# Kernel optimization log

Hardware: AMD Instinct MI355X
Metric: run time of the kernel (lower is better)

Reference implementation:

```python
import jax, jax.numpy as jnp
import numpy as np

DECAY = 0.99
EPS = 1e-05


def setup_inputs() -> dict:
    key = jax.random.key(0)
    k1, k2, k3 = jax.random.split(key, 3)
    N, K, D = 131072, 1024, 64
    return {
        "z": jax.random.normal(k1, (N, D), dtype=jnp.float32),
        "embeddings": jax.random.normal(k2, (K, D), dtype=jnp.float32),
        "cluster_size": jnp.ones((K,), dtype=jnp.float32),
        "ema_embed_sum": jax.random.normal(k3, (K, D), dtype=jnp.float32),
    }


def reference(z, embeddings, cluster_size, ema_embed_sum):
    # z: [N, D]; embeddings/ema_embed_sum: [K, D]; cluster_size: [K]
    N, D = z.shape
    K = embeddings.shape[0]

    # squared pairwise distances via the ||a||^2 - 2ab + ||b||^2 expansion
    d = (
        jnp.sum(z * z, axis=-1, keepdims=True)
        - 2.0 * (z @ embeddings.T)
        + jnp.sum(embeddings * embeddings, axis=-1)
    )  # [N, K]
    encoding_indices = jnp.argmin(d, axis=1)  # [N]
    z_q = embeddings[encoding_indices]  # [N, D]

    # EMA codebook update (training mode; one_hot.sum(0) == counts, one_hot.T @ z == segment_sum)
    counts = jax.ops.segment_sum(jnp.ones((N,), z.dtype), encoding_indices, num_segments=K)
    new_cluster_size = cluster_size * DECAY + (1.0 - DECAY) * counts
    embed_sum = jax.ops.segment_sum(z, encoding_indices, num_segments=K)  # [K, D]
    new_ema_embed_sum = ema_embed_sum * DECAY + (1.0 - DECAY) * embed_sum
    n = jnp.sum(new_cluster_size)
    cs = (new_cluster_size + EPS) / (n + K * EPS) * n
    new_embeddings = new_ema_embed_sum / cs[:, None]

    commitment_loss = jnp.mean((z - z_q) ** 2)
    z_q_st = z + jax.lax.stop_gradient(z_q - z)  # value == z_q
    return (z_q_st, commitment_loss, encoding_indices, new_embeddings, new_cluster_size, new_ema_embed_sum)
```

## Files before the change

### kernel.cpp

```cpp
#include <hip/hip_runtime.h>

#define N_PTS 131072
#define K_CODES 1024
#define DIM 64
#define DECAYF 0.99f
#define OMDF 0.01f
#define EPSF 1e-5f
#define TAU 0.0625f

#define OUT_ZQ      0
#define OUT_LOSS    8388608
#define OUT_IDX     8388609
#define OUT_NEWEMB  8519681
#define OUT_NEWCS   8585217
#define OUT_NEWEMA  8586241

#define WS_C8       0
#define WS_ACNT     8192
#define WS_EMBSUM   8208
#define WS_ZERO_END 73744
#define WS_ENORM    73744
#define WS_CNT      74768
#define WS_START    75792
#define WS_CUR8     76816
#define WS_LOSSARR  85008
#define WS_CS       85520
#define WS_AMBIG    86544
#define WS_ORDER    217616
#define WS_E2       348688

typedef __attribute__((ext_vector_type(8))) short bf16x8;
typedef __attribute__((ext_vector_type(4))) float f32x4;

static __device__ inline short f2bf(float f) {
    unsigned u = __float_as_uint(f);
    unsigned r = (u + 0x7fffu + ((u >> 16) & 1u)) >> 16;
    return (short)r;
}
static __device__ inline float bf2f(short h) {
    return __uint_as_float(((unsigned)(unsigned short)h) << 16);
}

__global__ __launch_bounds__(256) void econv_kernel(const float* __restrict__ E,
                                                    short* __restrict__ E2,
                                                    float* __restrict__ enorm) {
    int k = blockIdx.x * 256 + threadIdx.x;
    const float* ep = E + (size_t)k * DIM;
    short* o = E2 + (size_t)k * 128;
    float s = 0.f;
#pragma unroll
    for (int d = 0; d < 64; ++d) {
        float f = ep[d];
        s += f * f;
        float m = -2.f * f;
        short h = f2bf(m);
        o[d] = h;
        o[64 + d] = f2bf(m - bf2f(h));
    }
    enorm[k] = s;
}

__global__ __launch_bounds__(256) void argmin_mfma(const float* __restrict__ z,
                                                   const short* __restrict__ E2,
                                                   const float* __restrict__ enorm,
                                                   float* __restrict__ out_idx_f,
                                                   float* __restrict__ counts8,
                                                   int* __restrict__ ambig_cnt,
                                                   int* __restrict__ ambig) {
    int tid = threadIdx.x;
    int w = tid >> 6, lane = tid & 63;
    int c = lane & 15, q = lane >> 4;
    int mbase = blockIdx.x * 256 + w * 64;

    bf16x8 a[4][4];
#pragma unroll
    for (int t = 0; t < 4; ++t) {
        const float* zp = z + (size_t)(mbase + t * 16 + c) * DIM;
        const float4* z4a = (const float4*)(zp + q * 8);
        const float4* z4b = (const float4*)(zp + 32 + q * 8);
        float f[16];
        float4 v0 = z4a[0], v1 = z4a[1], v2 = z4b[0], v3 = z4b[1];
        f[0]=v0.x; f[1]=v0.y; f[2]=v0.z; f[3]=v0.w;
        f[4]=v1.x; f[5]=v1.y; f[6]=v1.z; f[7]=v1.w;
        f[8]=v2.x; f[9]=v2.y; f[10]=v2.z; f[11]=v2.w;
        f[12]=v3.x; f[13]=v3.y; f[14]=v3.z; f[15]=v3.w;
#pragma unroll
        for (int j = 0; j < 8; ++j) {
            short h0 = f2bf(f[j]);
            a[t][0][j] = h0;
            a[t][2][j] = f2bf(f[j] - bf2f(h0));
            short h1 = f2bf(f[8 + j]);
            a[t][1][j] = h1;
            a[t][3][j] = f2bf(f[8 + j] - bf2f(h1));
        }
    }

    float s1[16], s2[16];
    int i1[16];
#pragma unroll
    for (int idx = 0; idx < 16; ++idx) { s1[idx] = INFINITY; s2[idx] = INFINITY; i1[idx] = 0; }

    int vcode = c;
    for (int tile = 0; tile < 64; ++tile) {
        const bf16x8* bp = (const bf16x8*)E2 + ((size_t)(tile * 16 + c) * 16) + q;
        bf16x8 bh0 = bp[0], bh1 = bp[4], bl0 = bp[8], bl1 = bp[12];
        float en = enorm[tile * 16 + c];
#pragma unroll
        for (int t = 0; t < 4; ++t) {
            f32x4 acc = {0.f, 0.f, 0.f, 0.f};
            acc = __builtin_amdgcn_mfma_f32_16x16x32_bf16(a[t][0], bl0, acc, 0, 0, 0);
            acc = __builtin_amdgcn_mfma_f32_16x16x32_bf16(a[t][1], bl1, acc, 0, 0, 0);
            acc = __builtin_amdgcn_mfma_f32_16x16x32_bf16(a[t][2], bh0, acc, 0, 0, 0);
            acc = __builtin_amdgcn_mfma_f32_16x16x32_bf16(a[t][3], bh1, acc, 0, 0, 0);
            acc = __builtin_amdgcn_mfma_f32_16x16x32_bf16(a[t][0], bh0, acc, 0, 0, 0);
            acc = __builtin_amdgcn_mfma_f32_16x16x32_bf16(a[t][1], bh1, acc, 0, 0, 0);
#pragma unroll
            for (int i = 0; i < 4; ++i) {
                float s = en + acc[i];
                int idx = t * 4 + i;
                bool bl = s < s1[idx];
                s2[idx] = bl ? s1[idx] : fminf(s2[idx], s);
                i1[idx] = bl ? vcode : i1[idx];
                s1[idx] = bl ? s : s1[idx];
            }
        }
        vcode += 16;
    }

#pragma unroll
    for (int off = 1; off < 16; off <<= 1) {
#pragma unroll
        for (int idx = 0; idx < 16; ++idx) {
            float os1 = __shfl_xor(s1[idx], off);
            float os2 = __shfl_xor(s2[idx], off);
            int   oi1 = __shfl_xor(i1[idx], off);
            float ns2 = fminf(fmaxf(s1[idx], os1), fminf(s2[idx], os2));
            if (os1 < s1[idx]) { s1[idx] = os1; i1[idx] = oi1; }
            s2[idx] = ns2;
        }
    }

    if (c == 0) {
#pragma unroll
        for (int idx = 0; idx < 16; ++idx) {
            int t = idx >> 2, i = idx & 3;
            int row = mbase + t * 16 + q * 4 + i;
            int code = i1[idx];
            out_idx_f[row] = (float)code;
            if (s2[idx] - s1[idx] >= TAU) {
                atomicAdd(&counts8[(((unsigned)row >> 8) & 7) * K_CODES + code], 1.0f);
            } else {
                int p = atomicAdd(ambig_cnt, 1);
                ambig[p] = row;
            }
        }
    }
}

__global__ __launch_bounds__(256) void rescue_kernel(const float* __restrict__ z,
                                                     const float* __restrict__ E,
                                                     const float* __restrict__ enorm,
                                                     const int* __restrict__ ambig_cnt,
                                                     const int* __restrict__ ambig,
                                                     float* __restrict__ out_idx_f,
                                                     float* __restrict__ counts8) {
    int lane = threadIdx.x & 63;
    int wave = (blockIdx.x * 256 + threadIdx.x) >> 6;
    int nw = gridDim.x * 4;
    int cnt = *ambig_cnt;
    for (int a = 2 * wave; a < cnt; a += 2 * nw) {
        int row0 = ambig[a];
        bool two = (a + 1) < cnt;
        int row1 = two ? ambig[a + 1] : row0;
        const float4* zp0 = (const float4*)(z + (size_t)row0 * DIM);
        const float4* zp1 = (const float4*)(z + (size_t)row1 * DIM);
        float4 zr0[16], zr1[16];
#pragma unroll
        for (int i = 0; i < 16; ++i) { zr0[i] = zp0[i]; zr1[i] = zp1[i]; }
        float best0 = INFINITY, best1 = INFINITY;
        int bi0 = 0, bi1 = 0;
        for (int j = 0; j < 16; ++j) {
            int code = j * 64 + lane;
            const float4* ep = (const float4*)(E + (size_t)code * DIM);
            float a0 = 0.f, a1 = 0.f, a2 = 0.f, a3 = 0.f;
            float c0 = 0.f, c1 = 0.f, c2 = 0.f, c3 = 0.f;
#pragma unroll
            for (int i = 0; i < 16; ++i) {
                float4 ev = ep[i];
                a0 += zr0[i].x * ev.x; a1 += zr0[i].y * ev.y;
                a2 += zr0[i].z * ev.z; a3 += zr0[i].w * ev.w;
                c0 += zr1[i].x * ev.x; c1 += zr1[i].y * ev.y;
                c2 += zr1[i].z * ev.z; c3 += zr1[i].w * ev.w;
            }
            float en = enorm[code];
            float s0 = en - 2.f * ((a0 + a1) + (a2 + a3));
            float s1 = en - 2.f * ((c0 + c1) + (c2 + c3));
            if (s0 < best0) { best0 = s0; bi0 = code; }
            if (s1 < best1) { best1 = s1; bi1 = code; }
        }
#pragma unroll
        for (int off = 1; off < 64; off <<= 1) {
            float ob = __shfl_xor(best0, off);
            int oi = __shfl_xor(bi0, off);
            if (ob < best0 || (ob == best0 && oi < bi0)) { best0 = ob; bi0 = oi; }
            float ob1 = __shfl_xor(best1, off);
            int oi1 = __shfl_xor(bi1, off);
            if (ob1 < best1 || (ob1 == best1 && oi1 < bi1)) { best1 = ob1; bi1 = oi1; }
        }
        if (lane == 0) {
            out_idx_f[row0] = (float)bi0;
            atomicAdd(&counts8[(((unsigned)row0 >> 8) & 7) * K_CODES + bi0], 1.0f);
            if (two) {
                out_idx_f[row1] = (float)bi1;
                atomicAdd(&counts8[(((unsigned)row1 >> 8) & 7) * K_CODES + bi1], 1.0f);
            }
        }
    }
}

__global__ __launch_bounds__(256) void zq_loss_kernel(const float* __restrict__ z,
                                                      const float* __restrict__ E,
                                                      const float* __restrict__ idx_f,
                                                      float* __restrict__ zq,
                                                      float* __restrict__ lossarr) {
    __shared__ int s_k[256];
    __shared__ float red[256];
    int tid = threadIdx.x;
    int rbase = blockIdx.x * 256;
    s_k[tid] = (int)idx_f[rbase + tid];
    __syncthreads();
    float acc = 0.f;
    size_t ebase = (size_t)rbase * DIM;
    for (int it = 0; it < 64; ++it) {
        int le = it * 256 + tid;
        int rl = le >> 6, d = le & 63;
        float ev = E[(size_t)s_k[rl] * DIM + d];
        float zv = z[ebase + le];
        zq[ebase + le] = ev;
        float df = zv - ev;
        acc += df * df;
    }
    red[tid] = acc;
    __syncthreads();
    for (int st = 128; st > 0; st >>= 1) {
        if (tid < st) red[tid] += red[tid + st];
        __syncthreads();
    }
    if (tid == 0) lossarr[blockIdx.x] = red[0];
}

__global__ __launch_bounds__(1024) void scan_kernel(const float* __restrict__ cluster_size,
                                                    const float* __restrict__ counts8,
                                                    float* __restrict__ ncs_out,
                                                    float* __restrict__ cs_ws,
                                                    float* __restrict__ cnt_out,
                                                    int* __restrict__ start,
                                                    int* __restrict__ cursor8) {
    int k = threadIdx.x;
    float c8[8];
    float cnt = 0.f;
#pragma unroll
    for (int s = 0; s < 8; ++s) { c8[s] = counts8[s * K_CODES + k]; cnt += c8[s]; }
    cnt_out[k] = cnt;
    float ncs = cluster_size[k] * DECAYF + OMDF * cnt;
    ncs_out[k] = ncs;

    __shared__ float red[1024];
    __shared__ int pfx[1024];
    red[k] = ncs;
    pfx[k] = (int)cnt;
    __syncthreads();
    for (int st = 512; st > 0; st >>= 1) {
        if (k < st) red[k] += red[k + st];
        __syncthreads();
    }
    float n = red[0];
    cs_ws[k] = (ncs + EPSF) / (n + (float)K_CODES * EPSF) * n;

    int my = (int)cnt;
    for (int off = 1; off < 1024; off <<= 1) {
        int add = (k >= off) ? pfx[k - off] : 0;
        __syncthreads();
        pfx[k] += add;
        __syncthreads();
    }
    int excl = pfx[k] - my;
    start[k] = excl;
    int run = excl;
#pragma unroll
    for (int s = 0; s < 8; ++s) { cursor8[s * K_CODES + k] = run; run += (int)c8[s]; }
}

__global__ __launch_bounds__(256) void scatter_kernel(const float* __restrict__ idx_f,
                                                      int* __restrict__ cursor8,
                                                      int* __restrict__ order) {
    int row = blockIdx.x * 256 + threadIdx.x;
    int k = (int)idx_f[row];
    int shard = ((unsigned)row >> 8) & 7;
    int p = atomicAdd(&cursor8[shard * K_CODES + k], 1);
    order[p] = (k << 17) | row;
}

__global__ __launch_bounds__(256) void segsum_kernel(const float* __restrict__ z,
                                                     const int* __restrict__ order,
                                                     float* __restrict__ embsum) {
    int lane = threadIdx.x & 63;
    int w = threadIdx.x >> 6;
    int wave = blockIdx.x * 4 + w;
    int base = wave * 64;

    int my = order[base + lane];

    int cur = __shfl(my, 0, 64) >> 17;
    float sum = 0.f;
#pragma unroll 8
    for (int i = 0; i < 64; ++i) {
        int p = __shfl(my, i, 64);
        int row = p & 0x1FFFF;
        int code = p >> 17;
        float v = z[(size_t)row * DIM + lane];
        if (code != cur) {
            atomicAdd(&embsum[(size_t)cur * DIM + lane], sum);
            sum = 0.f;
            cur = code;
        }
        sum += v;
    }
    atomicAdd(&embsum[(size_t)cur * DIM + lane], sum);
}

__global__ __launch_bounds__(256) void ema2_kernel(const float* __restrict__ ema,
                                                   const float* __restrict__ embsum,
                                                   const float* __restrict__ cs_ws,
                                                   float* __restrict__ newema_out,
                                                   float* __restrict__ newemb_out) {
    int i = blockIdx.x * 256 + threadIdx.x;
    float nes = ema[i] * DECAYF + OMDF * embsum[i];
    newema_out[i] = nes;
    newemb_out[i] = nes / cs_ws[i >> 6];
}

__global__ __launch_bounds__(512) void finalize_kernel(const float* __restrict__ lossarr,
                                                       float* __restrict__ loss_out) {
    __shared__ float red[512];
    red[threadIdx.x] = lossarr[threadIdx.x];
    __syncthreads();
    for (int st = 256; st > 0; st >>= 1) {
        if (threadIdx.x < st) red[threadIdx.x] += red[threadIdx.x + st];
        __syncthreads();
    }
    if (threadIdx.x == 0)
        loss_out[0] = red[0] * (1.0f / ((float)N_PTS * (float)DIM));
}

extern "C" void kernel_launch(void* const* d_in, const int* in_sizes, int n_in,
                              void* d_out, int out_size, void* d_ws, size_t ws_size,
                              hipStream_t stream) {
    const float* z            = (const float*)d_in[0];
    const float* E            = (const float*)d_in[1];
    const float* cluster_size = (const float*)d_in[2];
    const float* ema          = (const float*)d_in[3];
    float* out = (float*)d_out;
    float* ws  = (float*)d_ws;

    hipMemsetAsync(ws, 0, (size_t)WS_ZERO_END * sizeof(float), stream);

    econv_kernel<<<4, 256, 0, stream>>>(E, (short*)(ws + WS_E2), ws + WS_ENORM);

    argmin_mfma<<<N_PTS / 256, 256, 0, stream>>>(z, (const short*)(ws + WS_E2),
                                                 ws + WS_ENORM,
                                                 out + OUT_IDX,
                                                 ws + WS_C8,
                                                 (int*)(ws + WS_ACNT),
                                                 (int*)(ws + WS_AMBIG));

    rescue_kernel<<<512, 256, 0, stream>>>(z, E, ws + WS_ENORM,
                                           (const int*)(ws + WS_ACNT),
                                           (const int*)(ws + WS_AMBIG),
                                           out + OUT_IDX,
                                           ws + WS_C8);

    zq_loss_kernel<<<N_PTS / 256, 256, 0, stream>>>(z, E, out + OUT_IDX,
                                                    out + OUT_ZQ,
                                                    ws + WS_LOSSARR);

    scan_kernel<<<1, 1024, 0, stream>>>(cluster_size, ws + WS_C8,
                                        out + OUT_NEWCS, ws + WS_CS,
                                        ws + WS_CNT,
                                        (int*)(ws + WS_START),
                                        (int*)(ws + WS_CUR8));

    scatter_kernel<<<N_PTS / 256, 256, 0, stream>>>(out + OUT_IDX,
                                                    (int*)(ws + WS_CUR8),
                                                    (int*)(ws + WS_ORDER));

    segsum_kernel<<<N_PTS / 256, 256, 0, stream>>>(z,
                                                   (const int*)(ws + WS_ORDER),
                                                   ws + WS_EMBSUM);

    ema2_kernel<<<K_CODES * DIM / 256, 256, 0, stream>>>(ema, ws + WS_EMBSUM,
                                                         ws + WS_CS,
                                                         out + OUT_NEWEMA,
                                                         out + OUT_NEWEMB);

    finalize_kernel<<<1, 512, 0, stream>>>(ws + WS_LOSSARR, out + OUT_LOSS);
}
```

Before: 263.1 us.

## Pack code index into distance bits, fuse loss into argmin, drop finalize

The argmin loop now packs the code index into the low 10 mantissa bits of each distance, folds the codebook norm into the MFMA accumulator init, and tracks the two smallest values with fmin/med3 instead of separate index selects. The commitment loss is computed as ||z||^2 plus the min distance inside argmin and rescue, summed with atomics, so the zq kernel no longer re-reads z and the finalize kernel is removed. The scan kernel switches to wave-shuffle prefix sums. The ambiguity threshold becomes magnitude-relative to cover the precision lost in the bit packing, and the loss is now derived from the bf16-split distance expansion, which risks numerical error.

```diff
diff --git a/kernel.cpp b/kernel.cpp
--- a/kernel.cpp
+++ b/kernel.cpp
@@ -6,7 +6,6 @@
 #define DECAYF 0.99f
 #define OMDF 0.01f
 #define EPSF 1e-5f
-#define TAU 0.0625f
 
 #define OUT_ZQ      0
 #define OUT_LOSS    8388608
@@ -17,17 +16,15 @@
 
 #define WS_C8       0
 #define WS_ACNT     8192
-#define WS_EMBSUM   8208
-#define WS_ZERO_END 73744
-#define WS_ENORM    73744
-#define WS_CNT      74768
-#define WS_START    75792
-#define WS_CUR8     76816
-#define WS_LOSSARR  85008
-#define WS_CS       85520
-#define WS_AMBIG    86544
-#define WS_ORDER    217616
-#define WS_E2       348688
+#define WS_LOSS     8208
+#define WS_EMBSUM   8224
+#define WS_ZERO_END 73760
+#define WS_ENORM    73760
+#define WS_CUR8     74784
+#define WS_CS       82976
+#define WS_AMBIG    84000
+#define WS_ORDER    215072
+#define WS_E2       346144
 
 typedef __attribute__((ext_vector_type(8))) short bf16x8;
 typedef __attribute__((ext_vector_type(4))) float f32x4;
@@ -66,13 +63,15 @@
                                                    float* __restrict__ out_idx_f,
                                                    float* __restrict__ counts8,
                                                    int* __restrict__ ambig_cnt,
-                                                   int* __restrict__ ambig) {
+                                                   int* __restrict__ ambig,
+                                                   float* __restrict__ loss_ws) {
     int tid = threadIdx.x;
     int w = tid >> 6, lane = tid & 63;
     int c = lane & 15, q = lane >> 4;
     int mbase = blockIdx.x * 256 + w * 64;
 
     bf16x8 a[4][4];
+    float znorm_t[4];
 #pragma unroll
     for (int t = 0; t < 4; ++t) {
         const float* zp = z + (size_t)(mbase + t * 16 + c) * DIM;
@@ -84,6 +83,12 @@
         f[4]=v1.x; f[5]=v1.y; f[6]=v1.z; f[7]=v1.w;
         f[8]=v2.x; f[9]=v2.y; f[10]=v2.z; f[11]=v2.w;
         f[12]=v3.x; f[13]=v3.y; f[14]=v3.z; f[15]=v3.w;
+        float zn = 0.f;
+#pragma unroll
+        for (int j = 0; j < 16; ++j) zn += f[j] * f[j];
+#pragma unroll
+        for (int off = 16; off < 64; off <<= 1) zn += __shfl_xor(zn, off);
+        znorm_t[t] = zn;
 #pragma unroll
         for (int j = 0; j < 8; ++j) {
             short h0 = f2bf(f[j]);
@@ -96,18 +101,17 @@
     }
 
     float s1[16], s2[16];
-    int i1[16];
-#pragma unroll
-    for (int idx = 0; idx < 16; ++idx) { s1[idx] = INFINITY; s2[idx] = INFINITY; i1[idx] = 0; }
-
-    int vcode = c;
+#pragma unroll
+    for (int idx = 0; idx < 16; ++idx) { s1[idx] = INFINITY; s2[idx] = INFINITY; }
+
+    unsigned vcode = (unsigned)c;
     for (int tile = 0; tile < 64; ++tile) {
         const bf16x8* bp = (const bf16x8*)E2 + ((size_t)(tile * 16 + c) * 16) + q;
         bf16x8 bh0 = bp[0], bh1 = bp[4], bl0 = bp[8], bl1 = bp[12];
         float en = enorm[tile * 16 + c];
 #pragma unroll
         for (int t = 0; t < 4; ++t) {
-            f32x4 acc = {0.f, 0.f, 0.f, 0.f};
+            f32x4 acc = {en, en, en, en};
             acc = __builtin_amdgcn_mfma_f32_16x16x32_bf16(a[t][0], bl0, acc, 0, 0, 0);
             acc = __builtin_amdgcn_mfma_f32_16x16x32_bf16(a[t][1], bl1, acc, 0, 0, 0);
             acc = __builtin_amdgcn_mfma_f32_16x16x32_bf16(a[t][2], bh0, acc, 0, 0, 0);
@@ -116,12 +120,12 @@
             acc = __builtin_amdgcn_mfma_f32_16x16x32_bf16(a[t][1], bh1, acc, 0, 0, 0);
 #pragma unroll
             for (int i = 0; i < 4; ++i) {
-                float s = en + acc[i];
+                float sp = __uint_as_float(
+                    (__float_as_uint(acc[i]) & 0xFFFFFC00u) | vcode);
                 int idx = t * 4 + i;
-                bool bl = s < s1[idx];
-                s2[idx] = bl ? s1[idx] : fminf(s2[idx], s);
-                i1[idx] = bl ? vcode : i1[idx];
-                s1[idx] = bl ? s : s1[idx];
+                float ns2 = __builtin_amdgcn_fmed3f(s1[idx], s2[idx], sp);
+                s1[idx] = fminf(s1[idx], sp);
+                s2[idx] = ns2;
             }
         }
         vcode += 16;
@@ -133,27 +137,48 @@
         for (int idx = 0; idx < 16; ++idx) {
             float os1 = __shfl_xor(s1[idx], off);
             float os2 = __shfl_xor(s2[idx], off);
-            int   oi1 = __shfl_xor(i1[idx], off);
-            float ns2 = fminf(fmaxf(s1[idx], os1), fminf(s2[idx], os2));
-            if (os1 < s1[idx]) { s1[idx] = os1; i1[idx] = oi1; }
-            s2[idx] = ns2;
-        }
-    }
-
+            float ns1 = fminf(s1[idx], os1);
+            s2[idx] = fminf(fmaxf(s1[idx], os1), fminf(s2[idx], os2));
+            s1[idx] = ns1;
+        }
+    }
+
+    float znr[16];
+#pragma unroll
+    for (int t = 0; t < 4; ++t)
+#pragma unroll
+        for (int i = 0; i < 4; ++i)
+            znr[t * 4 + i] = __shfl(znorm_t[t], (q << 4) | (q * 4 + i), 64);
+
+    __shared__ float lred[16];
+    float lsum = 0.f;
     if (c == 0) {
 #pragma unroll
         for (int idx = 0; idx < 16; ++idx) {
             int t = idx >> 2, i = idx & 3;
             int row = mbase + t * 16 + q * 4 + i;
-            int code = i1[idx];
+            unsigned b1 = __float_as_uint(s1[idx]);
+            int code = (int)(b1 & 1023u);
             out_idx_f[row] = (float)code;
-            if (s2[idx] - s1[idx] >= TAU) {
+            float s1v = __uint_as_float(b1 & 0xFFFFFC00u);
+            float gap = s2[idx] - s1[idx];
+            float tau = 0.008f + 8e-4f * (fabsf(s1[idx]) + fabsf(s2[idx]));
+            if (gap >= tau) {
                 atomicAdd(&counts8[(((unsigned)row >> 8) & 7) * K_CODES + code], 1.0f);
+                lsum += znr[idx] + s1v;
             } else {
                 int p = atomicAdd(ambig_cnt, 1);
                 ambig[p] = row;
             }
         }
+        lred[w * 4 + q] = lsum;
+    }
+    __syncthreads();
+    if (tid == 0) {
+        float tot = 0.f;
+#pragma unroll
+        for (int i = 0; i < 16; ++i) tot += lred[i];
+        atomicAdd(loss_ws, tot);
     }
 }
 
@@ -163,7 +188,8 @@
                                                      const int* __restrict__ ambig_cnt,
                                                      const int* __restrict__ ambig,
                                                      float* __restrict__ out_idx_f,
-                                                     float* __restrict__ counts8) {
+                                                     float* __restrict__ counts8,
+                                                     float* __restrict__ loss_ws) {
     int lane = threadIdx.x & 63;
     int wave = (blockIdx.x * 256 + threadIdx.x) >> 6;
     int nw = gridDim.x * 4;
@@ -175,8 +201,14 @@
         const float4* zp0 = (const float4*)(z + (size_t)row0 * DIM);
         const float4* zp1 = (const float4*)(z + (size_t)row1 * DIM);
         float4 zr0[16], zr1[16];
-#pragma unroll
-        for (int i = 0; i < 16; ++i) { zr0[i] = zp0[i]; zr1[i] = zp1[i]; }
+        float zn0 = 0.f, zn1 = 0.f;
+#pragma unroll
+        for (int i = 0; i < 16; ++i) {
+            float4 u = zp0[i], v = zp1[i];
+            zr0[i] = u; zr1[i] = v;
+            zn0 += u.x * u.x + u.y * u.y + u.z * u.z + u.w * u.w;
+            zn1 += v.x * v.x + v.y * v.y + v.z * v.z + v.w * v.w;
+        }
         float best0 = INFINITY, best1 = INFINITY;
         int bi0 = 0, bi1 = 0;
         for (int j = 0; j < 16; ++j) {
@@ -210,82 +242,79 @@
         if (lane == 0) {
             out_idx_f[row0] = (float)bi0;
             atomicAdd(&counts8[(((unsigned)row0 >> 8) & 7) * K_CODES + bi0], 1.0f);
+            float ladd = zn0 + best0;
             if (two) {
                 out_idx_f[row1] = (float)bi1;
                 atomicAdd(&counts8[(((unsigned)row1 >> 8) & 7) * K_CODES + bi1], 1.0f);
+                ladd += zn1 + best1;
             }
-        }
-    }
-}
-
-__global__ __launch_bounds__(256) void zq_loss_kernel(const float* __restrict__ z,
-                                                      const float* __restrict__ E,
-                                                      const float* __restrict__ idx_f,
-                                                      float* __restrict__ zq,
-                                                      float* __restrict__ lossarr) {
+            atomicAdd(loss_ws, ladd);
+        }
+    }
+}
+
+__global__ __launch_bounds__(256) void zq_write_kernel(const float* __restrict__ E,
+                                                       const float* __restrict__ idx_f,
+                                                       float* __restrict__ zq) {
     __shared__ int s_k[256];
-    __shared__ float red[256];
     int tid = threadIdx.x;
     int rbase = blockIdx.x * 256;
     s_k[tid] = (int)idx_f[rbase + tid];
     __syncthreads();
-    float acc = 0.f;
     size_t ebase = (size_t)rbase * DIM;
+#pragma unroll 4
     for (int it = 0; it < 64; ++it) {
         int le = it * 256 + tid;
         int rl = le >> 6, d = le & 63;
-        float ev = E[(size_t)s_k[rl] * DIM + d];
-        float zv = z[ebase + le];
-        zq[ebase + le] = ev;
-        float df = zv - ev;
-        acc += df * df;
-    }
-    red[tid] = acc;
-    __syncthreads();
-    for (int st = 128; st > 0; st >>= 1) {
-        if (tid < st) red[tid] += red[tid + st];
-        __syncthreads();
-    }
-    if (tid == 0) lossarr[blockIdx.x] = red[0];
+        zq[ebase + le] = E[(size_t)s_k[rl] * DIM + d];
+    }
 }
 
 __global__ __launch_bounds__(1024) void scan_kernel(const float* __restrict__ cluster_size,
                                                     const float* __restrict__ counts8,
                                                     float* __restrict__ ncs_out,
                                                     float* __restrict__ cs_ws,
-                                                    float* __restrict__ cnt_out,
-                                                    int* __restrict__ start,
                                                     int* __restrict__ cursor8) {
     int k = threadIdx.x;
+    int lane = k & 63, wv = k >> 6;
     float c8[8];
     float cnt = 0.f;
 #pragma unroll
     for (int s = 0; s < 8; ++s) { c8[s] = counts8[s * K_CODES + k]; cnt += c8[s]; }
-    cnt_out[k] = cnt;
     float ncs = cluster_size[k] * DECAYF + OMDF * cnt;
     ncs_out[k] = ncs;
 
-    __shared__ float red[1024];
-    __shared__ int pfx[1024];
-    red[k] = ncs;
-    pfx[k] = (int)cnt;
+    int v = (int)cnt;
+    int vs = v;
+#pragma unroll
+    for (int off = 1; off < 64; off <<= 1) {
+        int o = __shfl_up(vs, off, 64);
+        if (lane >= off) vs += o;
+    }
+    float fs = ncs;
+#pragma unroll
+    for (int off = 1; off < 64; off <<= 1) fs += __shfl_xor(fs, off);
+
+    __shared__ int wtot[16];
+    __shared__ float ftot[16];
+    __shared__ float nsh;
+    if (lane == 63) wtot[wv] = vs;
+    if (lane == 0) ftot[wv] = fs;
     __syncthreads();
-    for (int st = 512; st > 0; st >>= 1) {
-        if (k < st) red[k] += red[k + st];
-        __syncthreads();
-    }
-    float n = red[0];
+    if (k == 0) {
+        int run = 0; float fn = 0.f;
+#pragma unroll
+        for (int i = 0; i < 16; ++i) {
+            int t = wtot[i]; wtot[i] = run; run += t;
+            fn += ftot[i];
+        }
+        nsh = fn;
+    }
+    __syncthreads();
+    float n = nsh;
     cs_ws[k] = (ncs + EPSF) / (n + (float)K_CODES * EPSF) * n;
 
-    int my = (int)cnt;
-    for (int off = 1; off < 1024; off <<= 1) {
-        int add = (k >= off) ? pfx[k - off] : 0;
-        __syncthreads();
-        pfx[k] += add;
-        __syncthreads();
-    }
-    int excl = pfx[k] - my;
-    start[k] = excl;
+    int excl = vs - v + wtot[wv];
     int run = excl;
 #pragma unroll
     for (int s = 0; s < 8; ++s) { cursor8[s * K_CODES + k] = run; run += (int)c8[s]; }
@@ -332,25 +361,16 @@
 __global__ __launch_bounds__(256) void ema2_kernel(const float* __restrict__ ema,
                                                    const float* __restrict__ embsum,
                                                    const float* __restrict__ cs_ws,
+                                                   const float* __restrict__ loss_ws,
                                                    float* __restrict__ newema_out,
-                                                   float* __restrict__ newemb_out) {
+                                                   float* __restrict__ newemb_out,
+                                                   float* __restrict__ loss_out) {
     int i = blockIdx.x * 256 + threadIdx.x;
     float nes = ema[i] * DECAYF + OMDF * embsum[i];
     newema_out[i] = nes;
     newemb_out[i] = nes / cs_ws[i >> 6];
-}
-
-__global__ __launch_bounds__(512) void finalize_kernel(const float* __restrict__ lossarr,
-                                                       float* __restrict__ loss_out) {
-    __shared__ float red[512];
-    red[threadIdx.x] = lossarr[threadIdx.x];
-    __syncthreads();
-    for (int st = 256; st > 0; st >>= 1) {
-        if (threadIdx.x < st) red[threadIdx.x] += red[threadIdx.x + st];
-        __syncthreads();
-    }
-    if (threadIdx.x == 0)
-        loss_out[0] = red[0] * (1.0f / ((float)N_PTS * (float)DIM));
+    if (i == 0)
+        loss_out[0] = loss_ws[0] * (1.0f / ((float)N_PTS * (float)DIM));
 }
 
 extern "C" void kernel_launch(void* const* d_in, const int* in_sizes, int n_in,
@@ -372,22 +392,21 @@
                                                  out + OUT_IDX,
                                                  ws + WS_C8,
                                                  (int*)(ws + WS_ACNT),
-                                                 (int*)(ws + WS_AMBIG));
+                                                 (int*)(ws + WS_AMBIG),
+                                                 ws + WS_LOSS);
 
     rescue_kernel<<<512, 256, 0, stream>>>(z, E, ws + WS_ENORM,
                                            (const int*)(ws + WS_ACNT),
                                            (const int*)(ws + WS_AMBIG),
                                            out + OUT_IDX,
-                                           ws + WS_C8);
-
-    zq_loss_kernel<<<N_PTS / 256, 256, 0, stream>>>(z, E, out + OUT_IDX,
-                                                    out + OUT_ZQ,
-                                                    ws + WS_LOSSARR);
+                                           ws + WS_C8,
+                                           ws + WS_LOSS);
+
+    zq_write_kernel<<<N_PTS / 256, 256, 0, stream>>>(E, out + OUT_IDX,
+                                                     out + OUT_ZQ);
 
     scan_kernel<<<1, 1024, 0, stream>>>(cluster_size, ws + WS_C8,
                                         out + OUT_NEWCS, ws + WS_CS,
-                                        ws + WS_CNT,
-                                        (int*)(ws + WS_START),
                                         (int*)(ws + WS_CUR8));
 
     scatter_kernel<<<N_PTS / 256, 256, 0, stream>>>(out + OUT_IDX,
@@ -400,8 +419,8 @@
 
     ema2_kernel<<<K_CODES * DIM / 256, 256, 0, stream>>>(ema, ws + WS_EMBSUM,
                                                          ws + WS_CS,
+                                                         ws + WS_LOSS,
                                                          out + OUT_NEWEMA,
-                                                         out + OUT_NEWEMB);
-
-    finalize_kernel<<<1, 512, 0, stream>>>(ws + WS_LOSSARR, out + OUT_LOSS);
-}
+                                                         out + OUT_NEWEMB,
+                                                         out + OUT_LOSS);
+}
```

After: 249.0 us. -5.3%, faster.
